# Kernel optimization log

Measured on AMD Instinct MI355X. Metric: run time of the kernel, lower is better.

## Reference

```python
import jax, jax.numpy as jnp
import numpy as np

N_FIL, N_SUB = 13, 4
N_NODES = N_FIL * N_SUB  # 52
FEAT = 6
HID = 128
N_LAYERS = 3
BATCH = 4096


def build_microtubule_edges(nf=N_FIL, ns=N_SUB):
    edges = []
    for i in range(nf):
        for j in range(ns - 1):
            a = i * ns + j
            b = a + 1
            edges += [[a, b], [b, a]]
    for i in range(nf):
        for j in range(ns):
            a = i * ns + j
            l = ((i - 1) % nf) * ns + j
            edges += [[a, l], [l, a]]
            r = ((i + 1) % nf) * ns + j
            edges += [[a, r], [r, a]]
    return np.asarray(edges, dtype=np.int64).T  # (2, 286)


def setup_inputs() -> dict:
    key = jax.random.key(0)
    ks = jax.random.split(key, 10)
    inp = {
        "q_current": jax.random.normal(ks[0], (BATCH, N_FIL, N_SUB, FEAT), jnp.float32),
        "W_in": jax.random.normal(ks[1], (HID, FEAT), jnp.float32) * 0.3,
        "b_in": jax.random.normal(ks[2], (HID,), jnp.float32) * 0.02,
        "W_gnn": jax.random.normal(ks[3], (N_LAYERS, HID, HID), jnp.float32) * (1.0 / np.sqrt(HID)),
        "b_gnn": jax.random.normal(ks[4], (N_LAYERS, HID), jnp.float32) * 0.02,
        "W_d1": jax.random.normal(ks[5], (HID, HID), jnp.float32) * (1.0 / np.sqrt(HID)),
        "b_d1": jax.random.normal(ks[6], (HID,), jnp.float32) * 0.02,
        "W_d2": jax.random.normal(ks[7], (FEAT, HID), jnp.float32) * (1.0 / np.sqrt(HID)),
        "b_d2": jax.random.normal(ks[8], (FEAT,), jnp.float32) * 0.02,
        "edge_index": jnp.asarray(build_microtubule_edges()),
    }
    return inp


def reference(q_current, W_in, b_in, W_gnn, b_gnn, W_d1, b_d1, W_d2, b_d2, edge_index):
    B = q_current.shape[0]
    x0 = q_current.reshape(B, N_NODES, FEAT)

    # PyG GCNConv default: add self-loops, symmetric normalization.
    loops = jnp.arange(N_NODES, dtype=edge_index.dtype)
    src = jnp.concatenate([edge_index[0], loops])  # message source j
    dst = jnp.concatenate([edge_index[1], loops])  # aggregation target i
    deg = jax.ops.segment_sum(jnp.ones_like(dst, dtype=x0.dtype), dst,
                              num_segments=N_NODES)
    dinv = jax.lax.rsqrt(deg)  # deg >= 1 because of self-loops
    norm = (dinv[src] * dinv[dst])[None, :, None]  # (1, E, 1)

    # encoder (batched over B and nodes)
    x = jax.nn.relu(jnp.einsum('bnf,hf->bnh', x0, W_in) + b_in)

    for l in range(N_LAYERS):
        h = jnp.einsum('bnh,oh->bno', x, W_gnn[l])     # linear, no bias
        msg = h[:, src, :] * norm                      # gather + scale
        agg = jnp.zeros_like(h).at[:, dst, :].add(msg)  # scatter-add
        x = x + jax.nn.relu(agg + b_gnn[l])            # bias after agg, residual

    # decoder (Dropout is identity in eval)
    y = jax.nn.relu(jnp.einsum('bnh,oh->bno', x, W_d1) + b_d1)
    y = jnp.einsum('bnh,fh->bnf', y, W_d2) + b_d2
    return y.reshape(B, N_FIL, N_SUB, FEAT)
```

## Files before the change

kernel.cpp:

```cpp
#include <hip/hip_runtime.h>


typedef __attribute__((ext_vector_type(2)))  float  f32x2;
typedef __attribute__((ext_vector_type(4)))  float  f32x4;
typedef __attribute__((ext_vector_type(16))) float  f32x16;
typedef __attribute__((ext_vector_type(8)))  __bf16 bf16x8;

#define MFMA(a, b, c) __builtin_amdgcn_mfma_f32_32x32x16_bf16((a), (b), (c), 0, 0, 0)

#define QSTR 53
#define QP   (QSTR * 4)

struct bfpair { __bf16 h, l; };
__device__ __forceinline__ bfpair splitf(float f) {
    bfpair p;
    p.h = (__bf16)f;
    p.l = (__bf16)(f - (float)p.h);
    return p;
}

__global__ __launch_bounds__(256) void prep_w(
    const float* __restrict__ Wg, const float* __restrict__ Wd1,
    __bf16* __restrict__ ws)
{
    const int tid  = blockIdx.x * 256 + threadIdx.x;
    const int lane = tid & 31;
    const int hi   = (tid >> 5) & 1;
    const int ot   = (tid >> 6) & 3;
    const int kc   = (tid >> 8) & 7;
    const int L    = tid >> 11;
    const float* src = ((L < 3) ? (Wg + L * 16384) : Wd1)
                     + (ot * 32 + lane) * 128 + kc * 16 + hi * 8;
    const f32x4 v0 = *(const f32x4*)(src);
    const f32x4 v1 = *(const f32x4*)(src + 4);
    bf16x8 h8, l8;
    #pragma unroll
    for (int e = 0; e < 4; ++e) {
        bfpair p0 = splitf(v0[e]); h8[e]   = p0.h; l8[e]   = p0.l;
        bfpair p1 = splitf(v1[e]); h8[4+e] = p1.h; l8[4+e] = p1.l;
    }
    ((bf16x8*)ws)[tid]        = h8;
    ((bf16x8*)ws)[8192 + tid] = l8;
}

__global__ __launch_bounds__(128, 3) void mt_fwd(
    const float* __restrict__ q,   const float* __restrict__ Win, const float* __restrict__ bin,
    const float* __restrict__ bg,  const float* __restrict__ bd1,
    const float* __restrict__ Wd2, const float* __restrict__ bd2,
    const bf16x8* __restrict__ Ph, float* __restrict__ out)
{
    __shared__ __attribute__((aligned(16))) float hs[32 * QP];

    const int t    = threadIdx.x;
    const int nt   = t >> 6;
    const int l    = t & 63;
    const int lane = l & 31;
    const int hi   = l >> 5;
    const int n    = nt * 32 + lane;
    const int nc   = (n < 52) ? n : 0;
    const int samp = blockIdx.x;
    const bf16x8* Pl = Ph + 8192;

    const int wbase = n * 4 + hi * QP;
    const int rbase = nc * 4 + hi * 2 * QP;

    int nb[5]; float nw[5];
    {
        const int   fi = n >> 2, js = n & 3;
        const float dg = 5.f + (js > 0 ? 1.f : 0.f) + (js < 3 ? 1.f : 0.f);
        const float di = rsqrtf(dg);
        nb[0] = n;                          nw[0] = di * di;
        nb[1] = ((fi + 12) % 13) * 4 + js;  nw[1] = 2.f * di * di;
        nb[2] = ((fi + 1) % 13) * 4 + js;   nw[2] = 2.f * di * di;
        nb[3] = (js > 0) ? (n - 1) : 0;
        nw[3] = (js > 0) ? di * rsqrtf(6.f + (js > 1 ? 1.f : 0.f)) : 0.f;
        nb[4] = (js < 3) ? (n + 1) : 0;
        nw[4] = (js < 3) ? di * rsqrtf(6.f + (js < 2 ? 1.f : 0.f)) : 0.f;
        if (n >= 52) {
            #pragma unroll
            for (int c = 0; c < 5; ++c) { nb[c] = 0; nw[c] = 0.f; }
        }
    }
    int gb[5];
    #pragma unroll
    for (int c = 0; c < 5; ++c) gb[c] = nb[c] * 4 + hi * 2 * QP;

    bf16x8 bh[8], bl[8];

    {
        f32x4 z4; z4[0]=0.f; z4[1]=0.f; z4[2]=0.f; z4[3]=0.f;
        f32x4 u0 = z4, u1 = z4;
        if (hi == 0 && n < 52) {
            const float* qp = q + (samp * 52 + n) * 6;
            const f32x2 a = *(const f32x2*)(qp);
            const f32x2 b = *(const f32x2*)(qp + 2);
            const f32x2 c = *(const f32x2*)(qp + 4);
            u0[0]=a[0]; u0[1]=a[1]; u0[2]=b[0]; u0[3]=b[1]; u1[0]=c[0]; u1[1]=c[1];
        }
        bf16x8 qh, ql;
        #pragma unroll
        for (int e = 0; e < 4; ++e) {
            bfpair p0 = splitf(u0[e]); qh[e]   = p0.h; ql[e]   = p0.l;
            bfpair p1 = splitf(u1[e]); qh[4+e] = p1.h; ql[4+e] = p1.l;
        }

        #pragma unroll
        for (int ot = 0; ot < 4; ++ot) {
            f32x4 v0 = z4, v1 = z4;
            if (hi == 0) {
                const int o_r = ot * 32 + lane;
                const f32x2 a = *(const f32x2*)(Win + o_r * 6);
                const f32x2 b = *(const f32x2*)(Win + o_r * 6 + 2);
                const f32x2 c = *(const f32x2*)(Win + o_r * 6 + 4);
                v0[0]=a[0]; v0[1]=a[1]; v0[2]=b[0]; v0[3]=b[1]; v1[0]=c[0]; v1[1]=c[1];
            }
            bf16x8 ah, al;
            #pragma unroll
            for (int e = 0; e < 4; ++e) {
                bfpair p0 = splitf(v0[e]); ah[e]   = p0.h; al[e]   = p0.l;
                bfpair p1 = splitf(v1[e]); ah[4+e] = p1.h; al[4+e] = p1.l;
            }
            f32x16 acc;
            #pragma unroll
            for (int r = 0; r < 16; ++r) acc[r] = 0.f;
            acc = MFMA(ah, qh, acc);
            acc = MFMA(ah, ql, acc);
            acc = MFMA(al, qh, acc);
            if (n < 52) {
                #pragma unroll
                for (int j = 0; j < 4; ++j) {
                    const f32x4 bv = *(const f32x4*)(bin + ot * 32 + 8 * j + 4 * hi);
                    f32x4 v;
                    #pragma unroll
                    for (int e = 0; e < 4; ++e) v[e] = fmaxf(acc[4 * j + e] + bv[e], 0.f);
                    *(f32x4*)&hs[wbase + (ot * 8 + 2 * j) * QP] = v;
                }
            }
        }
    }
    __syncthreads();
    #pragma unroll
    for (int kc = 0; kc < 8; ++kc) {
        const f32x4 a0 = *(const f32x4*)&hs[rbase + (kc * 4 + 0) * QP];
        const f32x4 a1 = *(const f32x4*)&hs[rbase + (kc * 4 + 1) * QP];
        #pragma unroll
        for (int e = 0; e < 4; ++e) {
            bfpair p0 = splitf(a0[e]); bh[kc][e]   = p0.h; bl[kc][e]   = p0.l;
            bfpair p1 = splitf(a1[e]); bh[kc][4+e] = p1.h; bl[kc][4+e] = p1.l;
        }
    }
    __syncthreads();

    #pragma unroll 1
    for (int L = 0; L < 3; ++L) {
        const int fbase = L * 2048 + hi * 32 + lane;

        #pragma unroll
        for (int op = 0; op < 2; ++op) {
            f32x16 acc0, acc1;
            #pragma unroll
            for (int r = 0; r < 16; ++r) { acc0[r] = 0.f; acc1[r] = 0.f; }
            #pragma unroll
            for (int kc = 0; kc < 8; ++kc) {
                const int fk = fbase + kc * 256 + op * 128;
                const bf16x8 wh0 = Ph[fk];
                const bf16x8 wl0 = Pl[fk];
                const bf16x8 wh1 = Ph[fk + 64];
                const bf16x8 wl1 = Pl[fk + 64];
                acc0 = MFMA(wh0, bh[kc], acc0);
                acc1 = MFMA(wh1, bh[kc], acc1);
                acc0 = MFMA(wh0, bl[kc], acc0);
                acc1 = MFMA(wh1, bl[kc], acc1);
                acc0 = MFMA(wl0, bh[kc], acc0);
                acc1 = MFMA(wl1, bh[kc], acc1);
            }
            if (n < 52) {
                #pragma unroll
                for (int j = 0; j < 4; ++j) {
                    f32x4 v0 = { acc0[4*j+0], acc0[4*j+1], acc0[4*j+2], acc0[4*j+3] };
                    f32x4 v1 = { acc1[4*j+0], acc1[4*j+1], acc1[4*j+2], acc1[4*j+3] };
                    *(f32x4*)&hs[wbase + ((2*op)   * 8 + 2 * j) * QP] = v0;
                    *(f32x4*)&hs[wbase + ((2*op+1) * 8 + 2 * j) * QP] = v1;
                }
            }
        }
        __syncthreads();

        const float* bsrc = bg + L * 128;
        #pragma unroll
        for (int kc = 0; kc < 8; ++kc) {
            f32x4 t0, t1;
            #pragma unroll
            for (int e = 0; e < 4; ++e) { t0[e] = 0.f; t1[e] = 0.f; }
            #pragma unroll
            for (int c = 0; c < 5; ++c) {
                const f32x4 r0 = *(const f32x4*)&hs[gb[c] + (kc * 4 + 0) * QP];
                const f32x4 r1 = *(const f32x4*)&hs[gb[c] + (kc * 4 + 1) * QP];
                t0 += nw[c] * r0;
                t1 += nw[c] * r1;
            }
            const int f0 = kc * 16 + 8 * hi;
            const f32x4 b0 = *(const f32x4*)(bsrc + f0);
            const f32x4 b1 = *(const f32x4*)(bsrc + f0 + 4);
            #pragma unroll
            for (int e = 0; e < 4; ++e) {
                {
                    const float xo = (float)bh[kc][e] + (float)bl[kc][e];
                    const float xn = xo + fmaxf(t0[e] + b0[e], 0.f);
                    bfpair p = splitf(xn); bh[kc][e] = p.h; bl[kc][e] = p.l;
                }
                {
                    const float xo = (float)bh[kc][4+e] + (float)bl[kc][4+e];
                    const float xn = xo + fmaxf(t1[e] + b1[e], 0.f);
                    bfpair p = splitf(xn); bh[kc][4+e] = p.h; bl[kc][4+e] = p.l;
                }
            }
        }
        __syncthreads();
    }

    {
        const int fbase = 3 * 2048 + hi * 32 + lane;
        #pragma unroll
        for (int op = 0; op < 2; ++op) {
            f32x16 acc0, acc1;
            #pragma unroll
            for (int r = 0; r < 16; ++r) { acc0[r] = 0.f; acc1[r] = 0.f; }
            #pragma unroll
            for (int kc = 0; kc < 8; ++kc) {
                const int fk = fbase + kc * 256 + op * 128;
                const bf16x8 wh0 = Ph[fk];
                const bf16x8 wl0 = Pl[fk];
                const bf16x8 wh1 = Ph[fk + 64];
                const bf16x8 wl1 = Pl[fk + 64];
                acc0 = MFMA(wh0, bh[kc], acc0);
                acc1 = MFMA(wh1, bh[kc], acc1);
                acc0 = MFMA(wh0, bl[kc], acc0);
                acc1 = MFMA(wh1, bl[kc], acc1);
                acc0 = MFMA(wl0, bh[kc], acc0);
                acc1 = MFMA(wl1, bh[kc], acc1);
            }
            if (n < 52) {
                #pragma unroll
                for (int j = 0; j < 4; ++j) {
                    const f32x4 bv0 = *(const f32x4*)(bd1 + (2*op)   * 32 + 8 * j + 4 * hi);
                    const f32x4 bv1 = *(const f32x4*)(bd1 + (2*op+1) * 32 + 8 * j + 4 * hi);
                    f32x4 v0, v1;
                    #pragma unroll
                    for (int e = 0; e < 4; ++e) {
                        v0[e] = fmaxf(acc0[4 * j + e] + bv0[e], 0.f);
                        v1[e] = fmaxf(acc1[4 * j + e] + bv1[e], 0.f);
                    }
                    *(f32x4*)&hs[wbase + ((2*op)   * 8 + 2 * j) * QP] = v0;
                    *(f32x4*)&hs[wbase + ((2*op+1) * 8 + 2 * j) * QP] = v1;
                }
            }
        }
        __syncthreads();
        #pragma unroll
        for (int kc = 0; kc < 8; ++kc) {
            const f32x4 a0 = *(const f32x4*)&hs[rbase + (kc * 4 + 0) * QP];
            const f32x4 a1 = *(const f32x4*)&hs[rbase + (kc * 4 + 1) * QP];
            #pragma unroll
            for (int e = 0; e < 4; ++e) {
                bfpair p0 = splitf(a0[e]); bh[kc][e]   = p0.h; bl[kc][e]   = p0.l;
                bfpair p1 = splitf(a1[e]); bh[kc][4+e] = p1.h; bl[kc][4+e] = p1.l;
            }
        }
    }

    {
        f32x16 acc;
        #pragma unroll
        for (int r = 0; r < 16; ++r) acc[r] = 0.f;
        f32x4 z4; z4[0]=0.f; z4[1]=0.f; z4[2]=0.f; z4[3]=0.f;

        #pragma unroll
        for (int kc = 0; kc < 8; ++kc) {
            const int kb = kc * 16 + 8 * hi;
            f32x4 w0 = z4, w1 = z4;
            if (lane < 6) {
                const float* wp = Wd2 + lane * 128 + kb;
                w0 = *(const f32x4*)(wp);
                w1 = *(const f32x4*)(wp + 4);
            }
            bf16x8 ah, al;
            #pragma unroll
            for (int e = 0; e < 4; ++e) {
                bfpair p0 = splitf(w0[e]); ah[e]   = p0.h; al[e]   = p0.l;
                bfpair p1 = splitf(w1[e]); ah[4+e] = p1.h; al[4+e] = p1.l;
            }
            acc = MFMA(ah, bh[kc], acc);
            acc = MFMA(ah, bl[kc], acc);
            acc = MFMA(al, bh[kc], acc);
        }
        if (n < 52) {
            float* op = out + (samp * 52 + n) * 6;
            if (hi == 0) {
                #pragma unroll
                for (int r = 0; r < 4; ++r) op[r] = acc[r] + bd2[r];
            } else {
                #pragma unroll
                for (int r = 0; r < 2; ++r) op[4 + r] = acc[r] + bd2[4 + r];
            }
        }
    }
}

extern "C" void kernel_launch(void* const* d_in, const int* in_sizes, int n_in,
                              void* d_out, int out_size, void* d_ws, size_t ws_size,
                              hipStream_t stream) {
    (void)in_sizes; (void)n_in; (void)ws_size; (void)out_size;
    const float* q   = (const float*)d_in[0];
    const float* Win = (const float*)d_in[1];
    const float* bin = (const float*)d_in[2];
    const float* Wg  = (const float*)d_in[3];
    const float* bg  = (const float*)d_in[4];
    const float* Wd1 = (const float*)d_in[5];
    const float* bd1 = (const float*)d_in[6];
    const float* Wd2 = (const float*)d_in[7];
    const float* bd2 = (const float*)d_in[8];
    float* out = (float*)d_out;

    prep_w<<<32, 256, 0, stream>>>(Wg, Wd1, (__bf16*)d_ws);
    mt_fwd<<<4096, 128, 0, stream>>>(q, Win, bin, bg, bd1, Wd2, bd2,
                                     (const bf16x8*)d_ws, out);
}
```

Before: 159.4 us.

## Halve LDS buffer by splitting output tiles into two phases; encoder via permlane

Shared memory is halved to 16 planes, and each layer's 128 output features are processed in two halves. The second half's MFMA tiles are computed before the first half's aggregation and written after it, which adds barriers. The encoder output is converted straight into B-operand registers with v_permlane32_swap instead of a round trip through shared memory. Launch bounds are raised to 4 blocks per CU to raise occupancy, at the cost of extra syncs and register pressure from holding two accumulator tiles.

```diff
diff --git a/kernel.cpp b/kernel.cpp
--- a/kernel.cpp
+++ b/kernel.cpp
@@ -5,6 +5,7 @@
 typedef __attribute__((ext_vector_type(4)))  float  f32x4;
 typedef __attribute__((ext_vector_type(16))) float  f32x16;
 typedef __attribute__((ext_vector_type(8)))  __bf16 bf16x8;
+typedef __attribute__((ext_vector_type(4)))  unsigned int u32x4;
 
 #define MFMA(a, b, c) __builtin_amdgcn_mfma_f32_32x32x16_bf16((a), (b), (c), 0, 0, 0)
 
@@ -17,6 +18,29 @@
     p.h = (__bf16)f;
     p.l = (__bf16)(f - (float)p.h);
     return p;
+}
+__device__ __forceinline__ unsigned pk2(__bf16 a, __bf16 b) {
+    return (unsigned)__builtin_bit_cast(unsigned short, a)
+         | ((unsigned)__builtin_bit_cast(unsigned short, b) << 16);
+}
+
+template<int RB>
+__device__ __forceinline__ void d2b8(const f32x16 &v, bf16x8 &BH, bf16x8 &BL) {
+    __bf16 h[8], l[8];
+    #pragma unroll
+    for (int i = 0; i < 8; ++i) { bfpair p = splitf(v[RB + i]); h[i] = p.h; l[i] = p.l; }
+    unsigned ha0 = pk2(h[0], h[1]), ha1 = pk2(h[2], h[3]);
+    unsigned hb0 = pk2(h[4], h[5]), hb1 = pk2(h[6], h[7]);
+    unsigned la0 = pk2(l[0], l[1]), la1 = pk2(l[2], l[3]);
+    unsigned lb0 = pk2(l[4], l[5]), lb1 = pk2(l[6], l[7]);
+    asm("v_permlane32_swap_b32 %0, %1" : "+v"(ha0), "+v"(hb0));
+    asm("v_permlane32_swap_b32 %0, %1" : "+v"(la0), "+v"(lb0));
+    asm("v_permlane32_swap_b32 %0, %1" : "+v"(ha1), "+v"(hb1));
+    asm("v_permlane32_swap_b32 %0, %1" : "+v"(la1), "+v"(lb1));
+    u32x4 uh = { ha0, ha1, hb0, hb1 };
+    u32x4 ul = { la0, la1, lb0, lb1 };
+    BH = __builtin_bit_cast(bf16x8, uh);
+    BL = __builtin_bit_cast(bf16x8, ul);
 }
 
 __global__ __launch_bounds__(256) void prep_w(
@@ -43,13 +67,13 @@
     ((bf16x8*)ws)[8192 + tid] = l8;
 }
 
-__global__ __launch_bounds__(128, 3) void mt_fwd(
+__global__ __launch_bounds__(128, 4) void mt_fwd(
     const float* __restrict__ q,   const float* __restrict__ Win, const float* __restrict__ bin,
     const float* __restrict__ bg,  const float* __restrict__ bd1,
     const float* __restrict__ Wd2, const float* __restrict__ bd2,
     const bf16x8* __restrict__ Ph, float* __restrict__ out)
 {
-    __shared__ __attribute__((aligned(16))) float hs[32 * QP];
+    __shared__ __attribute__((aligned(16))) float hb[16 * QP];
 
     const int t    = threadIdx.x;
     const int nt   = t >> 6;
@@ -61,8 +85,8 @@
     const int samp = blockIdx.x;
     const bf16x8* Pl = Ph + 8192;
 
-    const int wbase = n * 4 + hi * QP;
-    const int rbase = nc * 4 + hi * 2 * QP;
+    const int wq = n * 4;
+    const int rq = nc * 4;
 
     int nb[5]; float nw[5];
     {
@@ -81,9 +105,9 @@
             for (int c = 0; c < 5; ++c) { nb[c] = 0; nw[c] = 0.f; }
         }
     }
-    int gb[5];
+    int gq[5];
     #pragma unroll
-    for (int c = 0; c < 5; ++c) gb[c] = nb[c] * 4 + hi * 2 * QP;
+    for (int c = 0; c < 5; ++c) gq[c] = nb[c] * 4;
 
     bf16x8 bh[8], bl[8];
 
@@ -126,82 +150,82 @@
             acc = MFMA(ah, qh, acc);
             acc = MFMA(ah, ql, acc);
             acc = MFMA(al, qh, acc);
-            if (n < 52) {
+            f32x16 v;
+            #pragma unroll
+            for (int j = 0; j < 4; ++j) {
+                const f32x4 bv = *(const f32x4*)(bin + ot * 32 + 8 * j + 4 * hi);
                 #pragma unroll
-                for (int j = 0; j < 4; ++j) {
-                    const f32x4 bv = *(const f32x4*)(bin + ot * 32 + 8 * j + 4 * hi);
-                    f32x4 v;
-                    #pragma unroll
-                    for (int e = 0; e < 4; ++e) v[e] = fmaxf(acc[4 * j + e] + bv[e], 0.f);
-                    *(f32x4*)&hs[wbase + (ot * 8 + 2 * j) * QP] = v;
-                }
-            }
-        }
-    }
-    __syncthreads();
-    #pragma unroll
-    for (int kc = 0; kc < 8; ++kc) {
-        const f32x4 a0 = *(const f32x4*)&hs[rbase + (kc * 4 + 0) * QP];
-        const f32x4 a1 = *(const f32x4*)&hs[rbase + (kc * 4 + 1) * QP];
-        #pragma unroll
-        for (int e = 0; e < 4; ++e) {
-            bfpair p0 = splitf(a0[e]); bh[kc][e]   = p0.h; bl[kc][e]   = p0.l;
-            bfpair p1 = splitf(a1[e]); bh[kc][4+e] = p1.h; bl[kc][4+e] = p1.l;
-        }
-    }
-    __syncthreads();
+                for (int e = 0; e < 4; ++e) v[4 * j + e] = fmaxf(acc[4 * j + e] + bv[e], 0.f);
+            }
+            d2b8<0>(v, bh[2 * ot],     bl[2 * ot]);
+            d2b8<8>(v, bh[2 * ot + 1], bl[2 * ot + 1]);
+        }
+    }
+
+    auto mmtile = [&](int fbase, int ot) {
+        f32x16 acc;
+        #pragma unroll
+        for (int r = 0; r < 16; ++r) acc[r] = 0.f;
+        #pragma unroll
+        for (int kc = 0; kc < 8; ++kc) {
+            const int fk = fbase + kc * 256 + ot * 64;
+            const bf16x8 wh = Ph[fk];
+            const bf16x8 wl = Pl[fk];
+            acc = MFMA(wh, bh[kc], acc);
+            acc = MFMA(wh, bl[kc], acc);
+            acc = MFMA(wl, bh[kc], acc);
+        }
+        return acc;
+    };
+    auto wrplanes = [&](const f32x16 &acc, int ot) {
+        if (n < 52) {
+            #pragma unroll
+            for (int j = 0; j < 4; ++j) {
+                f32x4 v = { acc[4*j+0], acc[4*j+1], acc[4*j+2], acc[4*j+3] };
+                *(f32x4*)&hb[((ot & 1) * 8 + 2 * j + hi) * QP + wq] = v;
+            }
+        }
+    };
+    auto wrplanesRelu = [&](const f32x16 &acc, int ot, const float* bsrc) {
+        if (n < 52) {
+            #pragma unroll
+            for (int j = 0; j < 4; ++j) {
+                const f32x4 bv = *(const f32x4*)(bsrc + ot * 32 + 8 * j + 4 * hi);
+                f32x4 v;
+                #pragma unroll
+                for (int e = 0; e < 4; ++e) v[e] = fmaxf(acc[4 * j + e] + bv[e], 0.f);
+                *(f32x4*)&hb[((ot & 1) * 8 + 2 * j + hi) * QP + wq] = v;
+            }
+        }
+    };
 
     #pragma unroll 1
     for (int L = 0; L < 3; ++L) {
         const int fbase = L * 2048 + hi * 32 + lane;
-
-        #pragma unroll
-        for (int op = 0; op < 2; ++op) {
-            f32x16 acc0, acc1;
-            #pragma unroll
-            for (int r = 0; r < 16; ++r) { acc0[r] = 0.f; acc1[r] = 0.f; }
-            #pragma unroll
-            for (int kc = 0; kc < 8; ++kc) {
-                const int fk = fbase + kc * 256 + op * 128;
-                const bf16x8 wh0 = Ph[fk];
-                const bf16x8 wl0 = Pl[fk];
-                const bf16x8 wh1 = Ph[fk + 64];
-                const bf16x8 wl1 = Pl[fk + 64];
-                acc0 = MFMA(wh0, bh[kc], acc0);
-                acc1 = MFMA(wh1, bh[kc], acc1);
-                acc0 = MFMA(wh0, bl[kc], acc0);
-                acc1 = MFMA(wh1, bl[kc], acc1);
-                acc0 = MFMA(wl0, bh[kc], acc0);
-                acc1 = MFMA(wl1, bh[kc], acc1);
-            }
-            if (n < 52) {
-                #pragma unroll
-                for (int j = 0; j < 4; ++j) {
-                    f32x4 v0 = { acc0[4*j+0], acc0[4*j+1], acc0[4*j+2], acc0[4*j+3] };
-                    f32x4 v1 = { acc1[4*j+0], acc1[4*j+1], acc1[4*j+2], acc1[4*j+3] };
-                    *(f32x4*)&hs[wbase + ((2*op)   * 8 + 2 * j) * QP] = v0;
-                    *(f32x4*)&hs[wbase + ((2*op+1) * 8 + 2 * j) * QP] = v1;
-                }
-            }
-        }
-        __syncthreads();
-
         const float* bsrc = bg + L * 128;
-        #pragma unroll
-        for (int kc = 0; kc < 8; ++kc) {
+
+        {
+            f32x16 a0 = mmtile(fbase, 0); wrplanes(a0, 0);
+            f32x16 a1 = mmtile(fbase, 1); wrplanes(a1, 1);
+        }
+        __syncthreads();
+
+        f32x16 a2 = mmtile(fbase, 2);
+        f32x16 a3 = mmtile(fbase, 3);
+
+        #pragma unroll
+        for (int kc = 0; kc < 4; ++kc) {
+            const int p0 = ((kc >> 1) & 1) * 8 + (kc & 1) * 4 + 2 * hi;
             f32x4 t0, t1;
             #pragma unroll
             for (int e = 0; e < 4; ++e) { t0[e] = 0.f; t1[e] = 0.f; }
             #pragma unroll
             for (int c = 0; c < 5; ++c) {
-                const f32x4 r0 = *(const f32x4*)&hs[gb[c] + (kc * 4 + 0) * QP];
-                const f32x4 r1 = *(const f32x4*)&hs[gb[c] + (kc * 4 + 1) * QP];
-                t0 += nw[c] * r0;
-                t1 += nw[c] * r1;
-            }
-            const int f0 = kc * 16 + 8 * hi;
-            const f32x4 b0 = *(const f32x4*)(bsrc + f0);
-            const f32x4 b1 = *(const f32x4*)(bsrc + f0 + 4);
+                t0 += nw[c] * *(const f32x4*)&hb[p0 * QP + gq[c]];
+                t1 += nw[c] * *(const f32x4*)&hb[(p0 + 1) * QP + gq[c]];
+            }
+            const f32x4 b0 = *(const f32x4*)(bsrc + kc * 16 + 8 * hi);
+            const f32x4 b1 = *(const f32x4*)(bsrc + kc * 16 + 8 * hi + 4);
             #pragma unroll
             for (int e = 0; e < 4; ++e) {
                 {
@@ -217,54 +241,74 @@
             }
         }
         __syncthreads();
+
+        wrplanes(a2, 2);
+        wrplanes(a3, 3);
+        __syncthreads();
+
+        #pragma unroll
+        for (int kc = 4; kc < 8; ++kc) {
+            const int p0 = ((kc >> 1) & 1) * 8 + (kc & 1) * 4 + 2 * hi;
+            f32x4 t0, t1;
+            #pragma unroll
+            for (int e = 0; e < 4; ++e) { t0[e] = 0.f; t1[e] = 0.f; }
+            #pragma unroll
+            for (int c = 0; c < 5; ++c) {
+                t0 += nw[c] * *(const f32x4*)&hb[p0 * QP + gq[c]];
+                t1 += nw[c] * *(const f32x4*)&hb[(p0 + 1) * QP + gq[c]];
+            }
+            const f32x4 b0 = *(const f32x4*)(bsrc + kc * 16 + 8 * hi);
+            const f32x4 b1 = *(const f32x4*)(bsrc + kc * 16 + 8 * hi + 4);
+            #pragma unroll
+            for (int e = 0; e < 4; ++e) {
+                {
+                    const float xo = (float)bh[kc][e] + (float)bl[kc][e];
+                    const float xn = xo + fmaxf(t0[e] + b0[e], 0.f);
+                    bfpair p = splitf(xn); bh[kc][e] = p.h; bl[kc][e] = p.l;
+                }
+                {
+                    const float xo = (float)bh[kc][4+e] + (float)bl[kc][4+e];
+                    const float xn = xo + fmaxf(t1[e] + b1[e], 0.f);
+                    bfpair p = splitf(xn); bh[kc][4+e] = p.h; bl[kc][4+e] = p.l;
+                }
+            }
+        }
+        __syncthreads();
     }
 
     {
         const int fbase = 3 * 2048 + hi * 32 + lane;
-        #pragma unroll
-        for (int op = 0; op < 2; ++op) {
-            f32x16 acc0, acc1;
-            #pragma unroll
-            for (int r = 0; r < 16; ++r) { acc0[r] = 0.f; acc1[r] = 0.f; }
-            #pragma unroll
-            for (int kc = 0; kc < 8; ++kc) {
-                const int fk = fbase + kc * 256 + op * 128;
-                const bf16x8 wh0 = Ph[fk];
-                const bf16x8 wl0 = Pl[fk];
-                const bf16x8 wh1 = Ph[fk + 64];
-                const bf16x8 wl1 = Pl[fk + 64];
-                acc0 = MFMA(wh0, bh[kc], acc0);
-                acc1 = MFMA(wh1, bh[kc], acc1);
-                acc0 = MFMA(wh0, bl[kc], acc0);
-                acc1 = MFMA(wh1, bl[kc], acc1);
-                acc0 = MFMA(wl0, bh[kc], acc0);
-                acc1 = MFMA(wl1, bh[kc], acc1);
-            }
-            if (n < 52) {
-                #pragma unroll
-                for (int j = 0; j < 4; ++j) {
-                    const f32x4 bv0 = *(const f32x4*)(bd1 + (2*op)   * 32 + 8 * j + 4 * hi);
-                    const f32x4 bv1 = *(const f32x4*)(bd1 + (2*op+1) * 32 + 8 * j + 4 * hi);
-                    f32x4 v0, v1;
-                    #pragma unroll
-                    for (int e = 0; e < 4; ++e) {
-                        v0[e] = fmaxf(acc0[4 * j + e] + bv0[e], 0.f);
-                        v1[e] = fmaxf(acc1[4 * j + e] + bv1[e], 0.f);
-                    }
-                    *(f32x4*)&hs[wbase + ((2*op)   * 8 + 2 * j) * QP] = v0;
-                    *(f32x4*)&hs[wbase + ((2*op+1) * 8 + 2 * j) * QP] = v1;
-                }
-            }
-        }
-        __syncthreads();
-        #pragma unroll
-        for (int kc = 0; kc < 8; ++kc) {
-            const f32x4 a0 = *(const f32x4*)&hs[rbase + (kc * 4 + 0) * QP];
-            const f32x4 a1 = *(const f32x4*)&hs[rbase + (kc * 4 + 1) * QP];
-            #pragma unroll
-            for (int e = 0; e < 4; ++e) {
-                bfpair p0 = splitf(a0[e]); bh[kc][e]   = p0.h; bl[kc][e]   = p0.l;
-                bfpair p1 = splitf(a1[e]); bh[kc][4+e] = p1.h; bl[kc][4+e] = p1.l;
+        {
+            f32x16 a0 = mmtile(fbase, 0); wrplanesRelu(a0, 0, bd1);
+            f32x16 a1 = mmtile(fbase, 1); wrplanesRelu(a1, 1, bd1);
+        }
+        __syncthreads();
+        f32x16 a2 = mmtile(fbase, 2);
+        f32x16 a3 = mmtile(fbase, 3);
+        #pragma unroll
+        for (int kc = 0; kc < 4; ++kc) {
+            const int p0 = ((kc >> 1) & 1) * 8 + (kc & 1) * 4 + 2 * hi;
+            const f32x4 a0r = *(const f32x4*)&hb[p0 * QP + rq];
+            const f32x4 a1r = *(const f32x4*)&hb[(p0 + 1) * QP + rq];
+            #pragma unroll
+            for (int e = 0; e < 4; ++e) {
+                bfpair q0 = splitf(a0r[e]); bh[kc][e]   = q0.h; bl[kc][e]   = q0.l;
+                bfpair q1 = splitf(a1r[e]); bh[kc][4+e] = q1.h; bl[kc][4+e] = q1.l;
+            }
+        }
+        __syncthreads();
+        wrplanesRelu(a2, 2, bd1);
+        wrplanesRelu(a3, 3, bd1);
+        __syncthreads();
+        #pragma unroll
+        for (int kc = 4; kc < 8; ++kc) {
+            const int p0 = ((kc >> 1) & 1) * 8 + (kc & 1) * 4 + 2 * hi;
+            const f32x4 a0r = *(const f32x4*)&hb[p0 * QP + rq];
+            const f32x4 a1r = *(const f32x4*)&hb[(p0 + 1) * QP + rq];
+            #pragma unroll
+            for (int e = 0; e < 4; ++e) {
+                bfpair q0 = splitf(a0r[e]); bh[kc][e]   = q0.h; bl[kc][e]   = q0.l;
+                bfpair q1 = splitf(a1r[e]); bh[kc][4+e] = q1.h; bl[kc][4+e] = q1.l;
             }
         }
     }
```

After: 614.0 us. 285% more time.
